# Performance work log

Hardware: AMD Instinct MI355X
Metric: run time of the kernel (lower is better)

Reference implementation:

```python
import jax, jax.numpy as jnp
import numpy as np

BN_EPS = 1e-5

def _sqdist(a, b):
    # a: (B,N,3), b: (B,M,3) -> (B,N,M)
    return (jnp.sum(a**2, -1)[:, :, None] + jnp.sum(b**2, -1)[:, None, :]
            - 2.0 * jnp.einsum('bnc,bmc->bnm', a, b))

def _knn_idx(pts, k):
    # smallest-k neighbor indices, (B,N,k)
    d = _sqdist(pts, pts)
    _, idx = jax.lax.top_k(-d, k)
    return idx

def _group(feat, idx):
    # feat (B,C,N), idx (B,N,K) -> (B,C,N,K)
    return jax.vmap(lambda f, i: f[:, i])(feat, idx)

def _gather_pts(pts, idx):
    # pts (B,M,C), idx (B,...) -> (B,...,C)
    return jax.vmap(lambda p, i: p[i])(pts, idx)

def _conv1(w, b, x):
    # 1x1 conv1d: w (O,C), x (B,C,N)
    return jnp.einsum('oc,bcn->bon', w, x) + b[None, :, None]

def _conv2(w, x, b=None):
    # 1x1 conv2d: w (O,C), x (B,C,N,K)
    y = jnp.einsum('oc,bcnk->bonk', w, x)
    return y if b is None else y + b[None, :, None, None]

def _bn_eval(x, gamma, beta):
    # eval-mode BatchNorm2d with running_mean=0, running_var=1
    s = gamma / jnp.sqrt(1.0 + BN_EPS)
    return x * s[None, :, None, None] + beta[None, :, None, None]

def _lgrp(x_q, x, P_anchor, map_idx, anchor_dist, lw1, lw2, lw3, k=16):
    # x_q, x: (B,n,3) -> weights (B,dim,n,k)
    d = _sqdist(x_q, x)
    _, idx = jax.lax.top_k(-d, k)                      # (B,n,k)
    neighbors = _gather_pts(x, idx)                    # (B,n,k,3)
    R1 = jnp.abs(x_q[:, :, None, :] - neighbors)       # (B,n,k,3)
    B_idx = _gather_pts(map_idx[..., None], idx)[..., 0]  # (B,n,k)
    anchorA = _gather_pts(P_anchor, map_idx)           # (B,n,3)
    anchorB = _gather_pts(P_anchor, B_idx)             # (B,n,k,3)
    dA = jnp.linalg.norm(x_q - anchorA, axis=-1)       # (B,n)
    dB = jnp.linalg.norm(neighbors - anchorB, axis=-1) # (B,n,k)
    dAB = jax.vmap(lambda ad, a, bi: ad[a[:, None], bi])(anchor_dist, map_idx, B_idx)
    R2s = dA[:, :, None] + dAB + dB                    # (B,n,k)
    R2 = jnp.broadcast_to(R2s[..., None], R1.shape)
    feats = jnp.concatenate([R1, R2], axis=-1).transpose(0, 3, 1, 2)  # (B,6,n,k)
    h = jax.nn.relu(_conv2(lw1, feats))
    h = jax.nn.relu(_conv2(lw2, h))
    return _conv2(lw3, h)                              # (B,dim,n,k)

def setup_inputs() -> dict:
    key = jax.random.key(0)
    ks = jax.random.split(key, 32)
    B, C_in, n, dim, M, k = 2, 128, 2048, 256, 128, 16
    hid_p, hid_a = 64, dim * 4
    s = 0.05
    inp = {
        'x': jax.random.normal(ks[0], (B, C_in, n), jnp.float32),
        'pos': jax.random.normal(ks[1], (B, 3, n), jnp.float32),
        'fps_idx': jax.random.randint(ks[2], (B, n), 0, n),
        'P_anchor': jax.random.normal(ks[3], (B, M, 3), jnp.float32),
        'map_idx': jax.random.randint(ks[4], (B, n), 0, M),
        'anchor_dist': jax.random.uniform(ks[5], (B, M, M), jnp.float32) * 2.0,
        'w_start': jax.random.normal(ks[6], (dim, C_in)) * s,
        'b_start': jnp.zeros((dim,), jnp.float32),
        'w_key': jax.random.normal(ks[7], (dim, dim)) * s,
        'b_key': jnp.zeros((dim,), jnp.float32),
        'w_query': jax.random.normal(ks[8], (dim, dim)) * s,
        'b_query': jnp.zeros((dim,), jnp.float32),
        'w_value': jax.random.normal(ks[9], (dim, dim)) * s,
        'b_value': jnp.zeros((dim,), jnp.float32),
        'pw1': jax.random.normal(ks[10], (hid_p, 3)) * s,
        'pb1': jnp.zeros((hid_p,), jnp.float32),
        'pg1': jnp.ones((hid_p,), jnp.float32),
        'pbt1': jnp.zeros((hid_p,), jnp.float32),
        'pw2': jax.random.normal(ks[11], (dim, hid_p)) * s,
        'pb2': jnp.zeros((dim,), jnp.float32),
        'lw1': jax.random.normal(ks[12], (32, 6)) * s,
        'lw2': jax.random.normal(ks[13], (64, 32)) * s,
        'lw3': jax.random.normal(ks[14], (dim, 64)) * s,
        'aw1': jax.random.normal(ks[15], (hid_a, dim)) * s,
        'ab1': jnp.zeros((hid_a,), jnp.float32),
        'ag1': jnp.ones((hid_a,), jnp.float32),
        'abt1': jnp.zeros((hid_a,), jnp.float32),
        'aw2': jax.random.normal(ks[16], (dim, hid_a)) * s,
        'ab2': jnp.zeros((dim,), jnp.float32),
        'w_end': jax.random.normal(ks[17], (C_in, dim)) * s,
        'b_end': jnp.zeros((C_in,), jnp.float32),
    }
    return inp

def reference(x, pos, fps_idx, P_anchor, map_idx, anchor_dist,
              w_start, b_start, w_key, b_key, w_query, b_query, w_value, b_value,
              pw1, pb1, pg1, pbt1, pw2, pb2, lw1, lw2, lw3,
              aw1, ab1, ag1, abt1, aw2, ab2, w_end, b_end):
    n_knn = 16
    identity = x
    xf = _conv1(w_start, b_start, x)                   # (B,dim,n)
    pos_f = pos.transpose(0, 2, 1)                     # (B,n,3)
    idx_knn = _knn_idx(pos_f, n_knn)                   # (B,n,k)
    key_f = _conv1(w_key, b_key, xf)
    value = _conv1(w_value, b_value, xf)
    query = _conv1(w_query, b_query, xf)
    key_g = _group(key_f, idx_knn)                     # (B,dim,n,k)
    qk_rel = query[:, :, :, None] - key_g
    pos_rel = pos[:, :, :, None] - _group(pos, idx_knn)
    f_l = _lgrp(pos_f, pos_f, P_anchor, map_idx, anchor_dist, lw1, lw2, lw3, k=16)
    # pos_mlp: conv-bn-relu-conv
    h = _bn_eval(_conv2(pw1, pos_rel, pb1), pg1, pbt1)
    pos_emb = _conv2(pw2, jax.nn.relu(h), pb2)         # (B,dim,n,k)
    # attn_mlp
    a = _bn_eval(_conv2(aw1, qk_rel + pos_emb + f_l, ab1), ag1, abt1)
    attention = _conv2(aw2, jax.nn.relu(a), ab2)
    attention = jax.nn.softmax(attention, axis=-1)
    value_e = value[:, :, :, None] + pos_emb + f_l
    agg = jnp.sum(attention * value_e, axis=-1)        # (B,dim,n)
    y = _conv1(w_end, b_end, agg)
    return y + identity
```

## Files before the change

kernel.cpp:

```cpp
#include <hip/hip_runtime.h>
#include <hip/hip_bf16.h>

typedef __hip_bfloat16 bf16;
typedef unsigned short u16;
typedef __attribute__((ext_vector_type(8))) short s8v;
typedef __attribute__((ext_vector_type(4))) float f32x4;

#define NP    2048
#define DC    256
#define MA    128
#define KNN_  16
#define LKV   768

#define MFMA_B16(a,b,c) __builtin_amdgcn_mfma_f32_16x16x32_bf16(a,b,c,0,0,0)

__device__ __forceinline__ float u2f(u16 u){ return __uint_as_float(((unsigned int)u)<<16); }
__device__ __forceinline__ u16 f2u(float f){ bf16 h=__float2bfloat16(f); u16 us; __builtin_memcpy(&us,&h,2); return us; }

__device__ __forceinline__ s8v ldpk(const u16* pk, int rb, int KS, int ks, int l){
  return *(const s8v*)(pk + (((size_t)((rb*KS + ks)*64 + l))<<3));
}

__device__ __forceinline__ s8v ldF(const u16* base, int cf, int ks, int NKS, int l){
  return *(const s8v*)((const char*)base + (((cf*NKS + ks)<<10) | (l<<4)));
}
__device__ __forceinline__ int faddr(int col, int ch, int NKS){
  int cf = col>>4, ks = ch>>5, lane = (((ch>>3)&3)<<4)|(col&15), j = ch&7;
  return ((cf*NKS + ks)<<10) + (lane<<4) + (j<<1);
}
__device__ __forceinline__ void stF4(u16* base, int col, int ch0, int NKS,
                                     float v0, float v1, float v2, float v3){
  uint2 pkv;
  pkv.x = (unsigned)f2u(v0) | ((unsigned)f2u(v1)<<16);
  pkv.y = (unsigned)f2u(v2) | ((unsigned)f2u(v3)<<16);
  *(uint2*)((char*)base + faddr(col, ch0, NKS)) = pkv;
}
__device__ __forceinline__ void stF1(u16* base, int col, int ch, int NKS, float v){
  *(u16*)((char*)base + faddr(col, ch, NKS)) = f2u(v);
}
__device__ __forceinline__ void ldF4(const u16* base, int col, int ch0, int NKS, float* o){
  uint2 pkv = *(const uint2*)((const char*)base + faddr(col, ch0, NKS));
  o[0] = u2f(pkv.x & 0xffff); o[1] = u2f(pkv.x>>16);
  o[2] = u2f(pkv.y & 0xffff); o[3] = u2f(pkv.y>>16);
}

__global__ __launch_bounds__(256) void kqv_fused(
    const u16* __restrict__ wstpk, const float* __restrict__ b_start,
    const u16* __restrict__ wkqvpk, const float* __restrict__ bkqv,
    const float* __restrict__ x, float* __restrict__ kqvT)
{
  __shared__ u16 Bx[64*128];
  __shared__ u16 Bt[64*256];
  const int tid = threadIdx.x;
  const int w = tid>>6, l = tid&63, k = l&15, g = l>>4;
  const int n0 = blockIdx.x*64, m0 = blockIdx.y*128, bb = blockIdx.z;
  for (int e = tid*4; e < 64*128; e += 1024) {
    int kk = e >> 6, c = e & 63;
    float4 v = *(const float4*)(x + (size_t)bb*128*NP + (size_t)kk*NP + n0 + c);
    stF1(Bx, c+0, kk, 4, v.x); stF1(Bx, c+1, kk, 4, v.y);
    stF1(Bx, c+2, kk, 4, v.z); stF1(Bx, c+3, kk, 4, v.w);
  }
  __syncthreads();
  {
    f32x4 accx[4][4];
#pragma unroll
    for (int fr = 0; fr < 4; fr++) {
      int ch0 = w*64 + fr*16 + g*4;
      float4 b4 = *(const float4*)(b_start + ch0);
#pragma unroll
      for (int cf = 0; cf < 4; cf++) {
        accx[fr][cf][0] = b4.x; accx[fr][cf][1] = b4.y;
        accx[fr][cf][2] = b4.z; accx[fr][cf][3] = b4.w;
      }
    }
#pragma unroll
    for (int ks = 0; ks < 4; ks++) {
      s8v aF[4];
#pragma unroll
      for (int fr = 0; fr < 4; fr++) aF[fr] = ldpk(wstpk, w*4 + fr, 4, ks, l);
#pragma unroll
      for (int cf = 0; cf < 4; cf++) {
        s8v bF = ldF(Bx, cf, ks, 4, l);
#pragma unroll
        for (int fr = 0; fr < 4; fr++) accx[fr][cf] = MFMA_B16(aF[fr], bF, accx[fr][cf]);
      }
    }
#pragma unroll
    for (int fr = 0; fr < 4; fr++)
#pragma unroll
      for (int cf = 0; cf < 4; cf++)
        stF4(Bt, cf*16 + k, w*64 + fr*16 + g*4, 8,
             accx[fr][cf][0], accx[fr][cf][1], accx[fr][cf][2], accx[fr][cf][3]);
  }
  __syncthreads();
  f32x4 acc[2][4] = {};
  const int rbase = (m0>>4) + w*2;
#pragma unroll
  for (int ks = 0; ks < 8; ks++) {
    s8v a0 = ldpk(wkqvpk, rbase,   8, ks, l);
    s8v a1 = ldpk(wkqvpk, rbase+1, 8, ks, l);
#pragma unroll
    for (int cf = 0; cf < 4; cf++) {
      s8v bF = ldF(Bt, cf, ks, 8, l);
      acc[0][cf] = MFMA_B16(a0, bF, acc[0][cf]);
      acc[1][cf] = MFMA_B16(a1, bF, acc[1][cf]);
    }
  }
#pragma unroll
  for (int ri = 0; ri < 2; ri++) {
    int mrow = m0 + w*32 + ri*16 + g*4;
#pragma unroll
    for (int r = 0; r < 4; r++) {
      int m = mrow + r;
      float bv = bkqv[m];
#pragma unroll
      for (int cf = 0; cf < 4; cf++) {
        int n = n0 + cf*16 + k;
        kqvT[((size_t)bb*NP + n)*LKV + m] = acc[ri][cf][r] + bv;
      }
    }
  }
}

template<bool XT, bool OT, bool RES>
__global__ __launch_bounds__(256) void mgemm(
    const u16* __restrict__ apk, const float* __restrict__ X,
    const float* __restrict__ bias, const float* __restrict__ resid,
    float* __restrict__ out, int M, int N, int K, int ldo)
{
  __shared__ u16 Bt[64*256];
  const int tid = threadIdx.x;
  const int w = tid>>6, l = tid&63, k = l&15, g = l>>4;
  const int n0 = blockIdx.x*64, m0 = blockIdx.y*128, bb = blockIdx.z;
  const int KS = K >> 5;
  if constexpr (!XT) {
    for (int e = tid*4; e < 64*K; e += 1024) {
      int kk = e >> 6, c = e & 63;
      float4 v = *(const float4*)(X + (size_t)bb*K*N + (size_t)kk*N + n0 + c);
      stF1(Bt, c+0, kk, KS, v.x); stF1(Bt, c+1, kk, KS, v.y);
      stF1(Bt, c+2, kk, KS, v.z); stF1(Bt, c+3, kk, KS, v.w);
    }
  } else {
    for (int e = tid*4; e < 64*256; e += 1024) {
      int c = e >> 8, kk = e & 255;
      float4 v = *(const float4*)(X + ((size_t)bb*N + n0 + c)*256 + kk);
      stF4(Bt, c, kk, KS, v.x, v.y, v.z, v.w);
    }
  }
  __syncthreads();
  f32x4 acc[2][4] = {};
  const int rbase = (m0>>4) + w*2;
  for (int ks = 0; ks < KS; ks++) {
    s8v a0 = ldpk(apk, rbase,   KS, ks, l);
    s8v a1 = ldpk(apk, rbase+1, KS, ks, l);
#pragma unroll
    for (int cf = 0; cf < 4; cf++) {
      s8v bF = ldF(Bt, cf, ks, KS, l);
      acc[0][cf] = MFMA_B16(a0, bF, acc[0][cf]);
      acc[1][cf] = MFMA_B16(a1, bF, acc[1][cf]);
    }
  }
#pragma unroll
  for (int ri = 0; ri < 2; ri++) {
    int mrow = m0 + w*32 + ri*16 + g*4;
#pragma unroll
    for (int r = 0; r < 4; r++) {
      int m = mrow + r;
      float bv = bias[m];
#pragma unroll
      for (int cf = 0; cf < 4; cf++) {
        int n = n0 + cf*16 + k;
        float v = acc[ri][cf][r] + bv;
        if constexpr (RES) v += resid[((size_t)bb*M + m)*N + n];
        if constexpr (OT) out[((size_t)bb*N + n)*ldo + m] = v;
        else              out[((size_t)bb*M + m)*N + n] = v;
      }
    }
  }
}

__global__ __launch_bounds__(1024) void knn_kernel(const float* __restrict__ pos, int* __restrict__ idx)
{
  __shared__ float px[NP], py[NP], pz[NP], pn[NP];
  const int tid = threadIdx.x;
  const int w = tid >> 6, l = tid & 63;
  const int bb = blockIdx.x >> 7;
  const int q0 = (blockIdx.x & 127) * 16;
  const float* pp = pos + (size_t)bb * 3 * NP;
  for (int t = tid; t < NP; t += 1024) {
    float x = pp[t], y = pp[NP + t], z = pp[2*NP + t];
    px[t] = x; py[t] = y; pz[t] = z; pn[t] = x*x + y*y + z*z;
  }
  __syncthreads();
  const int qi = q0 + w;
  const float qx = px[qi], qy = py[qi], qz = pz[qi], qn = pn[qi];
  float bd[16]; int bi[16];
#pragma unroll
  for (int t = 0; t < 16; t++) { bd[t] = 3.4e38f; bi[t] = -1; }
  float worst = 3.4e38f;
  for (int t = 0; t < 32; t++) {
    int j = t*64 + l;
    float d = qn + pn[j] - 2.f * (qx*px[j] + qy*py[j] + qz*pz[j]);
    if (__any(d < worst)) {
      float cd = (d < worst) ? d : 3.4e38f;
      int   cj = j;
#pragma unroll
      for (int s = 0; s < 16; s++) {
        bool sw = cd < bd[s];
        float od = bd[s]; int oj = bi[s];
        bd[s] = sw ? cd : od;  bi[s] = sw ? cj : oj;
        cd    = sw ? od : cd;  cj    = sw ? oj : cj;
      }
      worst = bd[15];
    }
  }
  int myj = 0;
#pragma unroll
  for (int r = 0; r < 16; r++) {
    float md = bd[0]; int mj = bi[0];
#pragma unroll
    for (int o = 1; o < 64; o <<= 1) {
      float od = __shfl_xor(md, o);
      int   oj = __shfl_xor(mj, o);
      bool tk = (od < md) || (od == md && ((unsigned)oj < (unsigned)mj));
      md = tk ? od : md;  mj = tk ? oj : mj;
    }
    if (l == r) myj = mj;
    bool win = (bi[0] == mj);
#pragma unroll
    for (int s = 0; s < 15; s++) {
      bd[s] = win ? bd[s+1] : bd[s];
      bi[s] = win ? bi[s+1] : bi[s];
    }
    bd[15] = win ? 3.4e38f : bd[15];
  }
  if (l < 16) idx[((size_t)bb * NP + qi) * KNN_ + l] = myj;
}

__global__ __launch_bounds__(256) void prep_kernel(
    const float* __restrict__ aw1, const float* __restrict__ aw2,
    const float* __restrict__ lw3, const float* __restrict__ pw2,
    const float* __restrict__ w_start, const float* __restrict__ w_key,
    const float* __restrict__ w_query, const float* __restrict__ w_value,
    const float* __restrict__ w_end,
    const float* __restrict__ b_key, const float* __restrict__ b_query,
    const float* __restrict__ b_value,
    const float* __restrict__ ag1, const float* __restrict__ ab1, const float* __restrict__ abt1,
    const float* __restrict__ pg1, const float* __restrict__ pb1, const float* __restrict__ pbt1,
    u16* __restrict__ aw1pk, u16* __restrict__ aw2pk, u16* __restrict__ wppk,
    u16* __restrict__ wstpk, u16* __restrict__ wkqvpk, u16* __restrict__ wendpk,
    float* __restrict__ sa, float* __restrict__ oa, float* __restrict__ sp,
    float* __restrict__ op_, float* __restrict__ bkqv)
{
  int i = blockIdx.x * 256 + threadIdx.x;
  const float inv = rsqrtf(1.0f + 1e-5f);
  if (i < 262144) {
    int rb = i >> 12, rem = i & 4095, ks = rem >> 9, l = (rem >> 3) & 63, j = rem & 7;
    int row = rb*16 + (l & 15), colk = ks*32 + (l >> 4)*8 + j;
    aw1pk[i] = f2u(aw1[(size_t)row*256 + colk]); return;
  }
  i -= 262144;
  if (i < 262144) {
    int rb = i >> 14, rem = i & 16383, ks = rem >> 9, l = (rem >> 3) & 63, j = rem & 7;
    int row = rb*16 + (l & 15), colk = ks*32 + (l >> 4)*8 + j;
    aw2pk[i] = f2u(aw2[(size_t)row*1024 + colk]); return;
  }
  i -= 262144;
  if (i < 32768) {
    int rb = i >> 11, rem = i & 2047, ks = rem >> 9, l = (rem >> 3) & 63, j = rem & 7;
    int row = rb*16 + (l & 15), colk = ks*32 + (l >> 4)*8 + j;
    float v = (colk < 64) ? lw3[row*64 + colk] : pw2[row*64 + (colk - 64)];
    wppk[i] = f2u(v); return;
  }
  i -= 32768;
  if (i < 32768) {
    int rb = i >> 11, rem = i & 2047, ks = rem >> 9, l = (rem >> 3) & 63, j = rem & 7;
    int row = rb*16 + (l & 15), colk = ks*32 + (l >> 4)*8 + j;
    wstpk[i] = f2u(w_start[(size_t)row*128 + colk]); return;
  }
  i -= 32768;
  if (i < 196608) {
    int rb = i >> 12, rem = i & 4095, ks = rem >> 9, l = (rem >> 3) & 63, j = rem & 7;
    int row = rb*16 + (l & 15), colk = ks*32 + (l >> 4)*8 + j;
    float v = (row < 256) ? w_key[(size_t)row*256 + colk]
            : (row < 512) ? w_query[(size_t)(row-256)*256 + colk]
                          : w_value[(size_t)(row-512)*256 + colk];
    wkqvpk[i] = f2u(v); return;
  }
  i -= 196608;
  if (i < 32768) {
    int rb = i >> 12, rem = i & 4095, ks = rem >> 9, l = (rem >> 3) & 63, j = rem & 7;
    int row = rb*16 + (l & 15), colk = ks*32 + (l >> 4)*8 + j;
    wendpk[i] = f2u(w_end[(size_t)row*256 + colk]); return;
  }
  i -= 32768;
  if (i < 1024) { float s_ = ag1[i]*inv; sa[i] = s_; oa[i] = ab1[i]*s_ + abt1[i]; return; }
  i -= 1024;
  if (i < 64)  { float s_ = pg1[i]*inv; sp[i] = s_; op_[i] = pb1[i]*s_ + pbt1[i]; return; }
  i -= 64;
  if (i < 768) {
    bkqv[i] = (i < 256) ? b_key[i] : (i < 512) ? b_query[i-256] : b_value[i-512];
  }
}

__global__ __launch_bounds__(256, 2) void fused_attn(
    const float* __restrict__ kqv, const int* __restrict__ knn_idx,
    const float* __restrict__ pos, const int* __restrict__ map_idx,
    const float* __restrict__ P_anchor, const float* __restrict__ adist,
    const float* __restrict__ lw1f, const float* __restrict__ lw2f, const float* __restrict__ pw1f,
    const float* __restrict__ spv, const float* __restrict__ opv, const float* __restrict__ pb2f,
    const u16* __restrict__ aw1pk, const float* __restrict__ sav, const float* __restrict__ oav,
    const u16* __restrict__ aw2pk, const u16* __restrict__ wppk, const float* __restrict__ ab2f,
    float* __restrict__ aggT)
{
  __shared__ __align__(16) char smem[65536];
  u16*   s_t   = (u16*)smem;
  u16*   hid0  = (u16*)(smem + 32768);
  u16*   hid1  = (u16*)(smem + 49152);
  float* fFEAT = (float*)smem;
  float* fPREL = (float*)(smem + 1632);
  u16*   fH1   = (u16*) (smem + 2448);

  const int tid = threadIdx.x;
  const int w = tid >> 6, l = tid & 63;
  const int k = l & 15, g = l >> 4;
  const int p0 = blockIdx.x * 4;
  const int b = p0 >> 11, pi0 = p0 & 2047;
  const int pi = pi0 + w;
  const int col_w = w*16 + k;

  const float* kqvB = kqv + (size_t)b * NP * LKV;
  const int* knnB = knn_idx + ((size_t)b * NP) * KNN_;

  if (l < 16) {
    int kk = l;
    int j = knnB[(size_t)pi * KNN_ + kk];
    const float* pp = pos + (size_t)b * 3 * NP;
    float qx = pp[pi], qy = pp[NP+pi], qz = pp[2*NP+pi];
    float nx = pp[j],  ny = pp[NP+j],  nz = pp[2*NP+j];
    float r1x = qx-nx, r1y = qy-ny, r1z = qz-nz;
    fPREL[(w*3+0)*17+kk] = r1x; fPREL[(w*3+1)*17+kk] = r1y; fPREL[(w*3+2)*17+kk] = r1z;
    int mi = map_idx[b*NP + pi];
    int bj = map_idx[b*NP + j];
    const float* pa = P_anchor + (size_t)b * MA * 3;
    float ax = pa[mi*3], ay = pa[mi*3+1], az = pa[mi*3+2];
    float bx = pa[bj*3], by = pa[bj*3+1], bz = pa[bj*3+2];
    float dA = sqrtf((qx-ax)*(qx-ax)+(qy-ay)*(qy-ay)+(qz-az)*(qz-az));
    float dB = sqrtf((nx-bx)*(nx-bx)+(ny-by)*(ny-by)+(nz-bz)*(nz-bz));
    float dAB = adist[(size_t)b*MA*MA + mi*MA + bj];
    float r2 = dA + dAB + dB;
    fFEAT[(w*6+0)*17+kk] = fabsf(r1x); fFEAT[(w*6+1)*17+kk] = fabsf(r1y);
    fFEAT[(w*6+2)*17+kk] = fabsf(r1z);
    fFEAT[(w*6+3)*17+kk] = r2; fFEAT[(w*6+4)*17+kk] = r2; fFEAT[(w*6+5)*17+kk] = r2;
  }
  __syncthreads();

  {
    float f0=fFEAT[(w*6+0)*17+k], f1=fFEAT[(w*6+1)*17+k], f2=fFEAT[(w*6+2)*17+k],
          f3=fFEAT[(w*6+3)*17+k], f4=fFEAT[(w*6+4)*17+k], f5=fFEAT[(w*6+5)*17+k];
#pragma unroll
    for (int jj = 0; jj < 8; jj++) {
      int h = g*8 + jj;
      const float* wp = lw1f + h*6;
      float v = wp[0]*f0 + wp[1]*f1 + wp[2]*f2 + wp[3]*f3 + wp[4]*f4 + wp[5]*f5;
      fH1[(w*32+h)*17+k] = f2u(fmaxf(v, 0.f));
    }
  }
  __syncthreads();

  {
    float hr[32];
#pragma unroll
    for (int t = 0; t < 32; t++) hr[t] = u2f(fH1[(w*32+t)*17+k]);
#pragma unroll
    for (int jj = 0; jj < 16; jj++) {
      int h = g*16 + jj;
      const float4* wp = (const float4*)(lw2f + h*32);
      float a = 0.f;
#pragma unroll
      for (int t4 = 0; t4 < 8; t4++) {
        float4 wv = wp[t4];
        a += wv.x*hr[t4*4] + wv.y*hr[t4*4+1] + wv.z*hr[t4*4+2] + wv.w*hr[t4*4+3];
      }
      stF1(hid0, col_w, h, 4, fmaxf(a, 0.f));
    }
    float pr0 = fPREL[(w*3+0)*17+k], pr1 = fPREL[(w*3+1)*17+k], pr2 = fPREL[(w*3+2)*17+k];
#pragma unroll
    for (int jj = 0; jj < 16; jj++) {
      int h = g*16 + jj;
      float d = pw1f[h*3]*pr0 + pw1f[h*3+1]*pr1 + pw1f[h*3+2]*pr2;
      stF1(hid0, col_w, 64 + h, 4, fmaxf(d*spv[h] + opv[h], 0.f));
    }
  }
  __syncthreads();

  {
    f32x4 accs[4][4];
#pragma unroll
    for (int fr = 0; fr < 4; fr++) {
      int ch0 = w*64 + fr*16 + g*4;
      const float4 p4 = *(const float4*)(pb2f + ch0);
#pragma unroll
      for (int fc = 0; fc < 4; fc++) {
        int j = knnB[(size_t)(pi0 + fc) * KNN_ + k];
        const float4 q4 = *(const float4*)(kqvB + (size_t)(pi0 + fc)*LKV + 256 + ch0);
        const float4 k4 = *(const float4*)(kqvB + (size_t)j*LKV + ch0);
        accs[fr][fc][0] = q4.x - k4.x + p4.x;
        accs[fr][fc][1] = q4.y - k4.y + p4.y;
        accs[fr][fc][2] = q4.z - k4.z + p4.z;
        accs[fr][fc][3] = q4.w - k4.w + p4.w;
      }
    }
#pragma unroll
    for (int ks = 0; ks < 4; ks++) {
      s8v aF[4];
#pragma unroll
      for (int fr = 0; fr < 4; fr++) aF[fr] = ldpk(wppk, w*4 + fr, 4, ks, l);
#pragma unroll
      for (int fc = 0; fc < 4; fc++) {
        s8v bF = ldF(hid0, fc, ks, 4, l);
#pragma unroll
        for (int fr = 0; fr < 4; fr++) accs[fr][fc] = MFMA_B16(aF[fr], bF, accs[fr][fc]);
      }
    }
#pragma unroll
    for (int fr = 0; fr < 4; fr++)
#pragma unroll
      for (int fc = 0; fc < 4; fc++)
        stF4(s_t, fc*16 + k, w*64 + fr*16 + g*4, 8,
             accs[fr][fc][0], accs[fr][fc][1], accs[fr][fc][2], accs[fr][fc][3]);
  }
  __syncthreads();

  f32x4 acc2[4][4];
#pragma unroll
  for (int fr = 0; fr < 4; fr++) {
    const float4 a4 = *(const float4*)(ab2f + w*64 + fr*16 + g*4);
#pragma unroll
    for (int fc = 0; fc < 4; fc++) {
      acc2[fr][fc][0] = a4.x; acc2[fr][fc][1] = a4.y;
      acc2[fr][fc][2] = a4.z; acc2[fr][fc][3] = a4.w;
    }
  }

  {
    f32x4 acc1[2][4] = {};
    const int rb0 = w*2;
    __builtin_amdgcn_s_setprio(1);
#pragma unroll
    for (int ks = 0; ks < 8; ks++) {
      s8v a0 = ldpk(aw1pk, rb0,     8, ks, l);
      s8v a1 = ldpk(aw1pk, rb0 + 1, 8, ks, l);
#pragma unroll
      for (int cf = 0; cf < 4; cf++) {
        s8v bF = ldF(s_t, cf, ks, 8, l);
        acc1[0][cf] = MFMA_B16(a0, bF, acc1[0][cf]);
        acc1[1][cf] = MFMA_B16(a1, bF, acc1[1][cf]);
      }
    }
    __builtin_amdgcn_s_setprio(0);
#pragma unroll
    for (int ri = 0; ri < 2; ri++) {
      int hl = w*32 + ri*16 + g*4;
      const float4 sc = *(const float4*)(sav + hl);
      const float4 of = *(const float4*)(oav + hl);
#pragma unroll
      for (int cf = 0; cf < 4; cf++) {
        float v0 = fmaxf(acc1[ri][cf][0]*sc.x + of.x, 0.f);
        float v1 = fmaxf(acc1[ri][cf][1]*sc.y + of.y, 0.f);
        float v2 = fmaxf(acc1[ri][cf][2]*sc.z + of.z, 0.f);
        float v3 = fmaxf(acc1[ri][cf][3]*sc.w + of.w, 0.f);
        stF4(hid0, cf*16 + k, hl, 4, v0, v1, v2, v3);
      }
    }
  }
  __syncthreads();

  for (int c = 0; c < 8; c++) {
    u16* cur = (c & 1) ? hid1 : hid0;
    u16* nxt = (c & 1) ? hid0 : hid1;
    __builtin_amdgcn_s_setprio(1);
#pragma unroll
    for (int ks = 0; ks < 4; ks++) {
      s8v aF[4];
#pragma unroll
      for (int rf = 0; rf < 4; rf++) aF[rf] = ldpk(aw2pk, w*4 + rf, 32, c*4 + ks, l);
#pragma unroll
      for (int cf = 0; cf < 4; cf++) {
        s8v bF = ldF(cur, cf, ks, 4, l);
#pragma unroll
        for (int rf = 0; rf < 4; rf++) acc2[rf][cf] = MFMA_B16(aF[rf], bF, acc2[rf][cf]);
      }
    }
    __builtin_amdgcn_s_setprio(0);
    if (c < 7) {
      f32x4 acc1[2][4] = {};
      const int rb0 = (c+1)*8 + w*2;
      __builtin_amdgcn_s_setprio(1);
#pragma unroll
      for (int ks = 0; ks < 8; ks++) {
        s8v a0 = ldpk(aw1pk, rb0,     8, ks, l);
        s8v a1 = ldpk(aw1pk, rb0 + 1, 8, ks, l);
#pragma unroll
        for (int cf = 0; cf < 4; cf++) {
          s8v bF = ldF(s_t, cf, ks, 8, l);
          acc1[0][cf] = MFMA_B16(a0, bF, acc1[0][cf]);
          acc1[1][cf] = MFMA_B16(a1, bF, acc1[1][cf]);
        }
      }
      __builtin_amdgcn_s_setprio(0);
#pragma unroll
      for (int ri = 0; ri < 2; ri++) {
        int hl = w*32 + ri*16 + g*4;
        int hg = (c+1)*128 + hl;
        const float4 sc = *(const float4*)(sav + hg);
        const float4 of = *(const float4*)(oav + hg);
#pragma unroll
        for (int cf = 0; cf < 4; cf++) {
          float v0 = fmaxf(acc1[ri][cf][0]*sc.x + of.x, 0.f);
          float v1 = fmaxf(acc1[ri][cf][1]*sc.y + of.y, 0.f);
          float v2 = fmaxf(acc1[ri][cf][2]*sc.z + of.z, 0.f);
          float v3 = fmaxf(acc1[ri][cf][3]*sc.w + of.w, 0.f);
          stF4(nxt, cf*16 + k, hl, 4, v0, v1, v2, v3);
        }
      }
      __syncthreads();
    }
  }

#pragma unroll
  for (int fc = 0; fc < 4; fc++) {
    int j = knnB[(size_t)(pi0 + fc) * KNN_ + k];
    const float* qp = kqvB + (size_t)(pi0 + fc)*LKV + 256;
    const float* kp = kqvB + (size_t)j*LKV;
    const float* vp = kqvB + (size_t)(pi0 + fc)*LKV + 512;
#pragma unroll
    for (int fr = 0; fr < 4; fr++) {
      int ch0 = w*64 + fr*16 + g*4;
      float q4[4], k4[4], v4[4], s4[4], res[4];
      *(float4*)q4 = *(const float4*)(qp + ch0);
      *(float4*)k4 = *(const float4*)(kp + ch0);
      *(float4*)v4 = *(const float4*)(vp + ch0);
      ldF4(s_t, fc*16 + k, ch0, 8, s4);
#pragma unroll
      for (int r = 0; r < 4; r++) {
        float a = acc2[fr][fc][r];
        float m = a;
        m = fmaxf(m, __shfl_xor(m, 1, 16)); m = fmaxf(m, __shfl_xor(m, 2, 16));
        m = fmaxf(m, __shfl_xor(m, 4, 16)); m = fmaxf(m, __shfl_xor(m, 8, 16));
        float ex = __expf(a - m);
        float se = ex;
        se += __shfl_xor(se, 1, 16); se += __shfl_xor(se, 2, 16);
        se += __shfl_xor(se, 4, 16); se += __shfl_xor(se, 8, 16);
        float watt = ex / se;
        float ve = v4[r] - q4[r] + k4[r] + s4[r];
        float cc = watt * ve;
        cc += __shfl_xor(cc, 1, 16); cc += __shfl_xor(cc, 2, 16);
        cc += __shfl_xor(cc, 4, 16); cc += __shfl_xor(cc, 8, 16);
        res[r] = cc;
      }
      if (k == 0)
        *(float4*)(aggT + ((size_t)(b*NP) + pi0 + fc)*DC + ch0) =
            make_float4(res[0], res[1], res[2], res[3]);
    }
  }
}

extern "C" void kernel_launch(void* const* d_in, const int* in_sizes, int n_in,
                              void* d_out, int out_size, void* d_ws, size_t ws_size,
                              hipStream_t stream)
{
  const float* x        = (const float*)d_in[0];
  const float* pos      = (const float*)d_in[1];
  const float* P_anchor = (const float*)d_in[3];
  const int*   map_idx  = (const int*)  d_in[4];
  const float* adist    = (const float*)d_in[5];
  const float* w_start  = (const float*)d_in[6];
  const float* b_start  = (const float*)d_in[7];
  const float* w_key    = (const float*)d_in[8];
  const float* b_key    = (const float*)d_in[9];
  const float* w_query  = (const float*)d_in[10];
  const float* b_query  = (const float*)d_in[11];
  const float* w_value  = (const float*)d_in[12];
  const float* b_value  = (const float*)d_in[13];
  const float* pw1      = (const float*)d_in[14];
  const float* pb1      = (const float*)d_in[15];
  const float* pg1      = (const float*)d_in[16];
  const float* pbt1     = (const float*)d_in[17];
  const float* pw2      = (const float*)d_in[18];
  const float* pb2      = (const float*)d_in[19];
  const float* lw1      = (const float*)d_in[20];
  const float* lw2      = (const float*)d_in[21];
  const float* lw3      = (const float*)d_in[22];
  const float* aw1      = (const float*)d_in[23];
  const float* ab1      = (const float*)d_in[24];
  const float* ag1      = (const float*)d_in[25];
  const float* abt1     = (const float*)d_in[26];
  const float* aw2      = (const float*)d_in[27];
  const float* ab2      = (const float*)d_in[28];
  const float* w_end    = (const float*)d_in[29];
  const float* b_end    = (const float*)d_in[30];

  if (ws_size < (size_t)4672384 * 4) return;

  float* ws     = (float*)d_ws;
  float* aggT   = ws + 0;
  float* kqvT   = ws + 1048576;
  u16*   aw1pk  = (u16*)(ws + 4194304);
  u16*   aw2pk  = (u16*)(ws + 4325376);
  u16*   wppk   = (u16*)(ws + 4456448);
  u16*   wstpk  = (u16*)(ws + 4472832);
  u16*   wkqvpk = (u16*)(ws + 4489216);
  u16*   wendpk = (u16*)(ws + 4587520);
  float* sa     = ws + 4603904;
  float* oa     = ws + 4604928;
  float* sp     = ws + 4605952;
  float* op_    = ws + 4606016;
  float* bkqv   = ws + 4606080;
  int*   knn_i  = (int*)(ws + 4606848);

  prep_kernel<<<3208, 256, 0, stream>>>(aw1, aw2, lw3, pw2,
      w_start, w_key, w_query, w_value, w_end, b_key, b_query, b_value,
      ag1, ab1, abt1, pg1, pb1, pbt1,
      aw1pk, aw2pk, wppk, wstpk, wkqvpk, wendpk, sa, oa, sp, op_, bkqv);

  knn_kernel<<<256, 1024, 0, stream>>>(pos, knn_i);

  kqv_fused<<<dim3(32, 6, 2), 256, 0, stream>>>(
      wstpk, b_start, wkqvpk, bkqv, x, kqvT);

  fused_attn<<<1024, 256, 0, stream>>>(kqvT, knn_i,
      pos, map_idx, P_anchor, adist,
      lw1, lw2, pw1, sp, op_, pb2,
      aw1pk, sa, oa, aw2pk, wppk, ab2, aggT);

  mgemm<true, false, true><<<dim3(32, 1, 2), 256, 0, stream>>>(
      wendpk, aggT, b_end, x, (float*)d_out, 128, NP, 256, 0);
}
```

Before: 209.2 us.

## Fuse end conv into attention kernel and merge weight prep with kNN

The final 1x1 conv plus bias and residual now runs inside fused_attn. Each block keeps its four aggregated points in shared memory and multiplies them by w_end with MFMA, so the aggT round trip through global memory and the separate mgemm launch are gone. The weight packing kernel and the kNN kernel are merged into one launch with 1024-thread blocks, which removes one more launch. In exchange, the end GEMM wastes most of its MFMA width on a 4-column tile (zero-padded to 16), and the prep blocks now reserve kNN-sized shared memory.

```diff
diff --git a/kernel.cpp b/kernel.cpp
--- a/kernel.cpp
+++ b/kernel.cpp
@@ -122,122 +122,8 @@
   }
 }
 
-template<bool XT, bool OT, bool RES>
-__global__ __launch_bounds__(256) void mgemm(
-    const u16* __restrict__ apk, const float* __restrict__ X,
-    const float* __restrict__ bias, const float* __restrict__ resid,
-    float* __restrict__ out, int M, int N, int K, int ldo)
-{
-  __shared__ u16 Bt[64*256];
-  const int tid = threadIdx.x;
-  const int w = tid>>6, l = tid&63, k = l&15, g = l>>4;
-  const int n0 = blockIdx.x*64, m0 = blockIdx.y*128, bb = blockIdx.z;
-  const int KS = K >> 5;
-  if constexpr (!XT) {
-    for (int e = tid*4; e < 64*K; e += 1024) {
-      int kk = e >> 6, c = e & 63;
-      float4 v = *(const float4*)(X + (size_t)bb*K*N + (size_t)kk*N + n0 + c);
-      stF1(Bt, c+0, kk, KS, v.x); stF1(Bt, c+1, kk, KS, v.y);
-      stF1(Bt, c+2, kk, KS, v.z); stF1(Bt, c+3, kk, KS, v.w);
-    }
-  } else {
-    for (int e = tid*4; e < 64*256; e += 1024) {
-      int c = e >> 8, kk = e & 255;
-      float4 v = *(const float4*)(X + ((size_t)bb*N + n0 + c)*256 + kk);
-      stF4(Bt, c, kk, KS, v.x, v.y, v.z, v.w);
-    }
-  }
-  __syncthreads();
-  f32x4 acc[2][4] = {};
-  const int rbase = (m0>>4) + w*2;
-  for (int ks = 0; ks < KS; ks++) {
-    s8v a0 = ldpk(apk, rbase,   KS, ks, l);
-    s8v a1 = ldpk(apk, rbase+1, KS, ks, l);
-#pragma unroll
-    for (int cf = 0; cf < 4; cf++) {
-      s8v bF = ldF(Bt, cf, ks, KS, l);
-      acc[0][cf] = MFMA_B16(a0, bF, acc[0][cf]);
-      acc[1][cf] = MFMA_B16(a1, bF, acc[1][cf]);
-    }
-  }
-#pragma unroll
-  for (int ri = 0; ri < 2; ri++) {
-    int mrow = m0 + w*32 + ri*16 + g*4;
-#pragma unroll
-    for (int r = 0; r < 4; r++) {
-      int m = mrow + r;
-      float bv = bias[m];
-#pragma unroll
-      for (int cf = 0; cf < 4; cf++) {
-        int n = n0 + cf*16 + k;
-        float v = acc[ri][cf][r] + bv;
-        if constexpr (RES) v += resid[((size_t)bb*M + m)*N + n];
-        if constexpr (OT) out[((size_t)bb*N + n)*ldo + m] = v;
-        else              out[((size_t)bb*M + m)*N + n] = v;
-      }
-    }
-  }
-}
-
-__global__ __launch_bounds__(1024) void knn_kernel(const float* __restrict__ pos, int* __restrict__ idx)
-{
-  __shared__ float px[NP], py[NP], pz[NP], pn[NP];
-  const int tid = threadIdx.x;
-  const int w = tid >> 6, l = tid & 63;
-  const int bb = blockIdx.x >> 7;
-  const int q0 = (blockIdx.x & 127) * 16;
-  const float* pp = pos + (size_t)bb * 3 * NP;
-  for (int t = tid; t < NP; t += 1024) {
-    float x = pp[t], y = pp[NP + t], z = pp[2*NP + t];
-    px[t] = x; py[t] = y; pz[t] = z; pn[t] = x*x + y*y + z*z;
-  }
-  __syncthreads();
-  const int qi = q0 + w;
-  const float qx = px[qi], qy = py[qi], qz = pz[qi], qn = pn[qi];
-  float bd[16]; int bi[16];
-#pragma unroll
-  for (int t = 0; t < 16; t++) { bd[t] = 3.4e38f; bi[t] = -1; }
-  float worst = 3.4e38f;
-  for (int t = 0; t < 32; t++) {
-    int j = t*64 + l;
-    float d = qn + pn[j] - 2.f * (qx*px[j] + qy*py[j] + qz*pz[j]);
-    if (__any(d < worst)) {
-      float cd = (d < worst) ? d : 3.4e38f;
-      int   cj = j;
-#pragma unroll
-      for (int s = 0; s < 16; s++) {
-        bool sw = cd < bd[s];
-        float od = bd[s]; int oj = bi[s];
-        bd[s] = sw ? cd : od;  bi[s] = sw ? cj : oj;
-        cd    = sw ? od : cd;  cj    = sw ? oj : cj;
-      }
-      worst = bd[15];
-    }
-  }
-  int myj = 0;
-#pragma unroll
-  for (int r = 0; r < 16; r++) {
-    float md = bd[0]; int mj = bi[0];
-#pragma unroll
-    for (int o = 1; o < 64; o <<= 1) {
-      float od = __shfl_xor(md, o);
-      int   oj = __shfl_xor(mj, o);
-      bool tk = (od < md) || (od == md && ((unsigned)oj < (unsigned)mj));
-      md = tk ? od : md;  mj = tk ? oj : mj;
-    }
-    if (l == r) myj = mj;
-    bool win = (bi[0] == mj);
-#pragma unroll
-    for (int s = 0; s < 15; s++) {
-      bd[s] = win ? bd[s+1] : bd[s];
-      bi[s] = win ? bi[s+1] : bi[s];
-    }
-    bd[15] = win ? 3.4e38f : bd[15];
-  }
-  if (l < 16) idx[((size_t)bb * NP + qi) * KNN_ + l] = myj;
-}
-
-__global__ __launch_bounds__(256) void prep_kernel(
+__global__ __launch_bounds__(1024) void prep_knn(
+    const float* __restrict__ pos, int* __restrict__ idx,
     const float* __restrict__ aw1, const float* __restrict__ aw2,
     const float* __restrict__ lw3, const float* __restrict__ pw2,
     const float* __restrict__ w_start, const float* __restrict__ w_key,
@@ -252,7 +138,64 @@
     float* __restrict__ sa, float* __restrict__ oa, float* __restrict__ sp,
     float* __restrict__ op_, float* __restrict__ bkqv)
 {
-  int i = blockIdx.x * 256 + threadIdx.x;
+  __shared__ float px[NP], py[NP], pz[NP], pn[NP];
+  if (blockIdx.x < 256) {
+    const int tid = threadIdx.x;
+    const int w = tid >> 6, l = tid & 63;
+    const int bb = blockIdx.x >> 7;
+    const int q0 = (blockIdx.x & 127) * 16;
+    const float* pp = pos + (size_t)bb * 3 * NP;
+    for (int t = tid; t < NP; t += 1024) {
+      float x = pp[t], y = pp[NP + t], z = pp[2*NP + t];
+      px[t] = x; py[t] = y; pz[t] = z; pn[t] = x*x + y*y + z*z;
+    }
+    __syncthreads();
+    const int qi = q0 + w;
+    const float qx = px[qi], qy = py[qi], qz = pz[qi], qn = pn[qi];
+    float bd[16]; int bi[16];
+#pragma unroll
+    for (int t = 0; t < 16; t++) { bd[t] = 3.4e38f; bi[t] = -1; }
+    float worst = 3.4e38f;
+    for (int t = 0; t < 32; t++) {
+      int j = t*64 + l;
+      float d = qn + pn[j] - 2.f * (qx*px[j] + qy*py[j] + qz*pz[j]);
+      if (__any(d < worst)) {
+        float cd = (d < worst) ? d : 3.4e38f;
+        int   cj = j;
+#pragma unroll
+        for (int s = 0; s < 16; s++) {
+          bool sw = cd < bd[s];
+          float od = bd[s]; int oj = bi[s];
+          bd[s] = sw ? cd : od;  bi[s] = sw ? cj : oj;
+          cd    = sw ? od : cd;  cj    = sw ? oj : cj;
+        }
+        worst = bd[15];
+      }
+    }
+    int myj = 0;
+#pragma unroll
+    for (int r = 0; r < 16; r++) {
+      float md = bd[0]; int mj = bi[0];
+#pragma unroll
+      for (int o = 1; o < 64; o <<= 1) {
+        float od = __shfl_xor(md, o);
+        int   oj = __shfl_xor(mj, o);
+        bool tk = (od < md) || (od == md && ((unsigned)oj < (unsigned)mj));
+        md = tk ? od : md;  mj = tk ? oj : mj;
+      }
+      if (l == r) myj = mj;
+      bool win = (bi[0] == mj);
+#pragma unroll
+      for (int s = 0; s < 15; s++) {
+        bd[s] = win ? bd[s+1] : bd[s];
+        bi[s] = win ? bi[s+1] : bi[s];
+      }
+      bd[15] = win ? 3.4e38f : bd[15];
+    }
+    if (l < 16) idx[((size_t)bb * NP + qi) * KNN_ + l] = myj;
+    return;
+  }
+  int i = (blockIdx.x - 256) * 1024 + threadIdx.x;
   const float inv = rsqrtf(1.0f + 1e-5f);
   if (i < 262144) {
     int rb = i >> 12, rem = i & 4095, ks = rem >> 9, l = (rem >> 3) & 63, j = rem & 7;
@@ -311,7 +254,8 @@
     const float* __restrict__ spv, const float* __restrict__ opv, const float* __restrict__ pb2f,
     const u16* __restrict__ aw1pk, const float* __restrict__ sav, const float* __restrict__ oav,
     const u16* __restrict__ aw2pk, const u16* __restrict__ wppk, const float* __restrict__ ab2f,
-    float* __restrict__ aggT)
+    const u16* __restrict__ wendpk, const float* __restrict__ b_endv,
+    const float* __restrict__ xin, float* __restrict__ outp)
 {
   __shared__ __align__(16) char smem[65536];
   u16*   s_t   = (u16*)smem;
@@ -528,6 +472,14 @@
     }
   }
 
+  {
+    uint2 z; z.x = 0u; z.y = 0u;
+    char* bz = (char*)hid0 + tid*32;
+#pragma unroll
+    for (int t = 0; t < 4; t++) *(uint2*)(bz + t*8) = z;
+  }
+  __syncthreads();
+
 #pragma unroll
   for (int fc = 0; fc < 4; fc++) {
     int j = knnB[(size_t)(pi0 + fc) * KNN_ + k];
@@ -553,15 +505,40 @@
         se += __shfl_xor(se, 1, 16); se += __shfl_xor(se, 2, 16);
         se += __shfl_xor(se, 4, 16); se += __shfl_xor(se, 8, 16);
         float watt = ex / se;
-        float ve = v4[r] - q4[r] + k4[r] + s4[r];
+        float ve = v4[r] - q4[r] + s4[r] + k4[r];
         float cc = watt * ve;
         cc += __shfl_xor(cc, 1, 16); cc += __shfl_xor(cc, 2, 16);
         cc += __shfl_xor(cc, 4, 16); cc += __shfl_xor(cc, 8, 16);
         res[r] = cc;
       }
       if (k == 0)
-        *(float4*)(aggT + ((size_t)(b*NP) + pi0 + fc)*DC + ch0) =
-            make_float4(res[0], res[1], res[2], res[3]);
+        stF4(hid0, fc, ch0, 8, res[0], res[1], res[2], res[3]);
+    }
+  }
+  __syncthreads();
+
+  {
+    f32x4 oacc[2] = {};
+#pragma unroll
+    for (int ks = 0; ks < 8; ks++) {
+      s8v a0 = ldpk(wendpk, w*2 + 0, 8, ks, l);
+      s8v a1 = ldpk(wendpk, w*2 + 1, 8, ks, l);
+      s8v bF = ldF(hid0, 0, ks, 8, l);
+      oacc[0] = MFMA_B16(a0, bF, oacc[0]);
+      oacc[1] = MFMA_B16(a1, bF, oacc[1]);
+    }
+    int p = l & 15;
+    if (p < 4) {
+      int g4 = l >> 4;
+#pragma unroll
+      for (int ri = 0; ri < 2; ri++) {
+#pragma unroll
+        for (int r = 0; r < 4; r++) {
+          int m = (w*2 + ri)*16 + g4*4 + r;
+          size_t o = ((size_t)(b*128) + m)*NP + pi0 + p;
+          outp[o] = oacc[ri][r] + b_endv[m] + xin[o];
+        }
+      }
     }
   }
 }
@@ -604,7 +581,6 @@
   if (ws_size < (size_t)4672384 * 4) return;
 
   float* ws     = (float*)d_ws;
-  float* aggT   = ws + 0;
   float* kqvT   = ws + 1048576;
   u16*   aw1pk  = (u16*)(ws + 4194304);
   u16*   aw2pk  = (u16*)(ws + 4325376);
@@ -619,12 +595,10 @@
   float* bkqv   = ws + 4606080;
   int*   knn_i  = (int*)(ws + 4606848);
 
-  prep_kernel<<<3208, 256, 0, stream>>>(aw1, aw2, lw3, pw2,
-      w_start, w_key, w_query, w_value, w_end, b_key, b_query, b_value,
-      ag1, ab1, abt1, pg1, pb1, pbt1,
+  prep_knn<<<1058, 1024, 0, stream>>>(pos, knn_i,
+      aw1, aw2, lw3, pw2, w_start, w_key, w_query, w_value, w_end,
+      b_key, b_query, b_value, ag1, ab1, abt1, pg1, pb1, pbt1,
       aw1pk, aw2pk, wppk, wstpk, wkqvpk, wendpk, sa, oa, sp, op_, bkqv);
-
-  knn_kernel<<<256, 1024, 0, stream>>>(pos, knn_i);
 
   kqv_fused<<<dim3(32, 6, 2), 256, 0, stream>>>(
       wstpk, b_start, wkqvpk, bkqv, x, kqvT);
@@ -632,8 +606,6 @@
   fused_attn<<<1024, 256, 0, stream>>>(kqvT, knn_i,
       pos, map_idx, P_anchor, adist,
       lw1, lw2, pw1, sp, op_, pb2,
-      aw1pk, sa, oa, aw2pk, wppk, ab2, aggT);
-
-  mgemm<true, false, true><<<dim3(32, 1, 2), 256, 0, stream>>>(
-      wendpk, aggT, b_end, x, (float*)d_out, 128, NP, 256, 0);
-}
+      aw1pk, sa, oa, aw2pk, wppk, ab2,
+      wendpk, b_end, x, (float*)d_out);
+}
```

After: 198.8 us, median of 2. 5.0% less time.
